# Kernel optimization log

Hardware: AMD Instinct MI355X
Metric: run time of the kernel (lower is better)

## Reference

```python
import jax, jax.numpy as jnp
import numpy as np

ROI_SIZE = 14  # hard-coded in the torch module


def _bilinear(feature, x, y):
    """feature: [B,C,H,W]; x, y: arbitrary (matching) shape S of sample coords.
    Returns [B, C, *S]. Matches torch code: corner indices are clamped BEFORE
    the interpolation weights are computed from them."""
    H, W = feature.shape[-2:]
    y1 = jnp.clip(jnp.floor(y).astype(jnp.int32), 0, H - 1)
    y2 = jnp.clip(jnp.floor(y).astype(jnp.int32) + 1, 0, H - 1)
    x1 = jnp.clip(jnp.floor(x).astype(jnp.int32), 0, W - 1)
    x2 = jnp.clip(jnp.floor(x).astype(jnp.int32) + 1, 0, W - 1)
    wx_lo = x - x1  # weight toward x2 column
    wx_hi = x2 - x  # weight toward x1 column
    wy_lo = y - y1
    wy_hi = y2 - y
    p = feature[:, :, y1, x1] * wx_hi + feature[:, :, y1, x2] * wx_lo
    q = feature[:, :, y2, x1] * wx_hi + feature[:, :, y2, x2] * wx_lo
    return p * wy_hi + q * wy_lo


def setup_inputs() -> dict:
    key = jax.random.key(0)
    kf, k1, k2, k3, k4 = jax.random.split(key, 5)
    B, C, H, W, R = 1, 256, 200, 320, 128
    feature = jax.random.normal(kf, (B, C, H, W), dtype=jnp.float32)
    y1 = jax.random.uniform(k1, (R,), minval=0.0, maxval=H * 0.5)
    x1 = jax.random.uniform(k2, (R,), minval=0.0, maxval=W * 0.5)
    hh = jax.random.uniform(k3, (R,), minval=8.0, maxval=H * 0.45)
    ww = jax.random.uniform(k4, (R,), minval=8.0, maxval=W * 0.45)
    rois = jnp.stack([y1, x1, y1 + hh, x1 + ww], axis=-1).astype(jnp.float32)
    return {"feature": feature, "rois": rois}


def reference(feature, rois):
    R = rois.shape[0]
    B, C, H, W = feature.shape
    sh = (rois[:, 2] - rois[:, 0]) / ROI_SIZE  # [R] bin height stride
    sw = (rois[:, 3] - rois[:, 1]) / ROI_SIZE  # [R] bin width stride
    m = jnp.arange(ROI_SIZE, dtype=rois.dtype)
    y_base = rois[:, 0:1] + sh[:, None] * m  # [R, M]
    x_base = rois[:, 1:2] + sw[:, None] * m  # [R, N]
    frac = jnp.array([1.0 / 3.0, 2.0 / 3.0], dtype=rois.dtype)
    ys = y_base[:, :, None] + sh[:, None, None] * frac  # [R, M, 2]
    xs = x_base[:, :, None] + sw[:, None, None] * frac  # [R, N, 2]
    # all 4 (y, x) sample-point combos per bin -> [R, M, N, 2, 2]
    yy = jnp.broadcast_to(ys[:, :, None, :, None], (R, ROI_SIZE, ROI_SIZE, 2, 2))
    xx = jnp.broadcast_to(xs[:, None, :, None, :], (R, ROI_SIZE, ROI_SIZE, 2, 2))
    samples = _bilinear(feature, xx, yy)  # [B, C, R, M, N, 2, 2]
    # Faithful to torch.max(tensor) with NO dim: global max over B, C, R and
    # the 4 sample points, giving one scalar per bin (m, n).
    bin_max = jnp.max(samples, axis=(0, 1, 2, 5, 6))  # [M, N]
    return jnp.broadcast_to(bin_max, (R, C, ROI_SIZE, ROI_SIZE))
```

## Files before the change

kernel.cpp:

```cpp
#include <hip/hip_runtime.h>
#include <float.h>

#define CC 256
#define HH 200
#define WW 320
#define HW (HH * WW)
#define MM 14
#define SPAN 148
#define NCH 8
#define CG 2
#define CPB (CC / CG)
#define ROUNDS (CPB / NCH)

typedef __attribute__((address_space(1))) const float GF;
typedef __attribute__((address_space(3))) float LF;

__global__ void roi_init(float* __restrict__ binmax) {
    int t = blockIdx.x * blockDim.x + threadIdx.x;
    if (t < MM * MM) binmax[t] = -FLT_MAX;
}

__device__ inline void atomicMaxF(float* addr, float val) {
    if (val >= 0.0f) {
        atomicMax((int*)addr, __float_as_int(val));
    } else {
        atomicMin((unsigned int*)addr, __float_as_uint(val));
    }
}

__global__ __launch_bounds__(256, 4) void roi_reduce(
    const float* __restrict__ feature,
    const float* __restrict__ rois,
    float* __restrict__ binmax)
{
    __shared__ float tile[2][NCH][4][SPAN];
    __shared__ float pmax[4][MM];

    const int bid = blockIdx.x;
    const int cg  = bid & (CG - 1);
    const int rm  = bid >> 1;
    const int m   = rm % MM;
    const int r   = rm / MM;
    const int tid  = threadIdx.x;
    const int w    = tid >> 6;
    const int lane = tid & 63;
    const int cbase = cg * CPB;

    const float ry1 = rois[r * 4 + 0];
    const float rx1 = rois[r * 4 + 1];
    const float ry2 = rois[r * 4 + 2];
    const float rx2 = rois[r * 4 + 3];
    const float sh = (ry2 - ry1) * (1.0f / 14.0f);
    const float sw = (rx2 - rx1) * (1.0f / 14.0f);
    const float f13 = 1.0f / 3.0f, f23 = 2.0f / 3.0f;

    const float yA = ry1 + sh * (float)m + sh * f13;
    const float yB = ry1 + sh * (float)m + sh * f23;
    const int y1A = min(max((int)floorf(yA), 0), HH - 1);
    const int y2A = min(max((int)floorf(yA) + 1, 0), HH - 1);
    const int y1B = min(max((int)floorf(yB), 0), HH - 1);
    const int y2B = min(max((int)floorf(yB) + 1, 0), HH - 1);
    const float wyloA = yA - (float)y1A, wyhiA = (float)y2A - yA;
    const float wyloB = yB - (float)y1B, wyhiB = (float)y2B - yB;

    const float xmin = rx1 + sw * f13;
    const float xmax = rx1 + sw * 13.0f + sw * f23;
    const int xlo = (min(max((int)floorf(xmin), 0), WW - 1)) & ~3;
    const int xhi = min(max((int)floorf(xmax) + 1, 0), WW - 1);
    int span = xhi - xlo + 1;
    if (span > SPAN) span = SPAN;
    const int nlanes = (span + 3) >> 2;

    const int myrow = (w == 0) ? y1A : (w == 1) ? y2A : (w == 2) ? y1B : y2B;
    const float* gbase = feature + (cbase * HW + myrow * WW + xlo) + lane * 4;

    const bool active = lane < 56;
    const int n = lane >> 2;
    const int j = (lane >> 1) & 1;
    const int i = lane & 1;

    float wxlo = 0.f, wxhi = 0.f, wylo = 0.f, wyhi = 0.f;
    int c0 = 0, ra = 0;
    if (active) {
        float x = rx1 + sw * (float)n + sw * (j ? f23 : f13);
        int x1c = min(max((int)floorf(x), 0), WW - 1);
        int x2c = min(max((int)floorf(x) + 1, 0), WW - 1);
        wxlo = x - (float)x1c;
        wxhi = (float)x2c - x;
        c0 = min(max(x1c - xlo, 0), SPAN - 2);
        if (i == 0) { ra = 0; wylo = wyloA; wyhi = wyhiA; }
        else        { ra = 2; wylo = wyloB; wyhi = wyhiB; }
    }

    auto stage = [&](int rd, int b) {
        const float* g = gbase + rd * (NCH * HW);
        if (lane < nlanes) {
            #pragma unroll
            for (int ch = 0; ch < NCH; ++ch) {
                __builtin_amdgcn_global_load_lds(
                    (GF*)(g + ch * HW), (LF*)&tile[b][ch][w][0], 16, 0, 0);
            }
        }
    };

    stage(0, 0);
    float lmax = -FLT_MAX;
    int buf = 0;

    for (int rd = 0; rd < ROUNDS; ++rd) {
        __syncthreads();
        if (rd + 1 < ROUNDS) stage(rd + 1, buf ^ 1);
        if (active) {
            #pragma unroll
            for (int q = 0; q < 2; ++q) {
                const float* rp = &tile[buf][w * 2 + q][ra][0];
                float v11 = rp[c0];
                float v12 = rp[c0 + 1];
                float v21 = rp[SPAN + c0];
                float v22 = rp[SPAN + c0 + 1];
                float p  = v11 * wxhi + v12 * wxlo;
                float qq = v21 * wxhi + v22 * wxlo;
                lmax = fmaxf(lmax, p * wyhi + qq * wylo);
            }
        }
        buf ^= 1;
    }

    float v = lmax;
    v = fmaxf(v, __shfl_xor(v, 1));
    v = fmaxf(v, __shfl_xor(v, 2));
    if (active && (lane & 3) == 0) pmax[w][n] = v;
    __syncthreads();
    if (tid < MM) {
        float vv = fmaxf(fmaxf(pmax[0][tid], pmax[1][tid]),
                         fmaxf(pmax[2][tid], pmax[3][tid]));
        atomicMaxF(&binmax[m * MM + tid], vv);
    }
}

__global__ __launch_bounds__(256) void roi_bcast(
    const float* __restrict__ binmax, float4* __restrict__ out, int total4)
{
    __shared__ float4 b4[49];
    int t = threadIdx.x;
    if (t < 49) b4[t] = ((const float4*)binmax)[t];
    __syncthreads();
    int idx = blockIdx.x * 256 + t;
    if (idx < total4) out[idx] = b4[idx % 49];
}

extern "C" void kernel_launch(void* const* d_in, const int* in_sizes, int n_in,
                              void* d_out, int out_size, void* d_ws, size_t ws_size,
                              hipStream_t stream) {
    const float* feature = (const float*)d_in[0];
    const float* rois    = (const float*)d_in[1];
    float* binmax = (float*)d_ws;
    float* out    = (float*)d_out;

    const int R = in_sizes[1] / 4;

    roi_init<<<1, 256, 0, stream>>>(binmax);
    roi_reduce<<<R * MM * CG, 256, 0, stream>>>(feature, rois, binmax);

    const int total4 = out_size / 4;
    roi_bcast<<<(total4 + 255) / 256, 256, 0, stream>>>(binmax, (float4*)out, total4);
}
```

Baseline: 165.4 us.

## Give each wave private channel slices and pipeline with waitcnt instead of barriers

Each wave now handles its own strided set of 64 channels and loads all four sample rows into a private double-buffered LDS tile. This replaces block-wide __syncthreads with per-wave s_waitcnt vmcnt/lgkmcnt fences. The channel-group split across blocks is removed, which halves the grid and makes each block do more work. The aim is to drop barrier stalls and let the waves stream independently, at the cost of fewer blocks, less occupancy and reliance on hand-written counter fencing.

```diff
diff --git a/kernel.cpp b/kernel.cpp
--- a/kernel.cpp
+++ b/kernel.cpp
@@ -6,11 +6,9 @@
 #define WW 320
 #define HW (HH * WW)
 #define MM 14
-#define SPAN 148
-#define NCH 8
-#define CG 2
-#define CPB (CC / CG)
-#define ROUNDS (CPB / NCH)
+#define SPAN 152
+#define NB 2
+#define CPW 64
 
 typedef __attribute__((address_space(1))) const float GF;
 typedef __attribute__((address_space(3))) float LF;
@@ -28,23 +26,20 @@
     }
 }
 
-__global__ __launch_bounds__(256, 4) void roi_reduce(
+__global__ __launch_bounds__(256) void roi_reduce(
     const float* __restrict__ feature,
     const float* __restrict__ rois,
     float* __restrict__ binmax)
 {
-    __shared__ float tile[2][NCH][4][SPAN];
+    __shared__ float tile[4][NB][4][SPAN];
     __shared__ float pmax[4][MM];
 
     const int bid = blockIdx.x;
-    const int cg  = bid & (CG - 1);
-    const int rm  = bid >> 1;
-    const int m   = rm % MM;
-    const int r   = rm / MM;
+    const int m   = bid % MM;
+    const int r   = bid / MM;
     const int tid  = threadIdx.x;
     const int w    = tid >> 6;
     const int lane = tid & 63;
-    const int cbase = cg * CPB;
 
     const float ry1 = rois[r * 4 + 0];
     const float rx1 = rois[r * 4 + 1];
@@ -71,8 +66,11 @@
     if (span > SPAN) span = SPAN;
     const int nlanes = (span + 3) >> 2;
 
-    const int myrow = (w == 0) ? y1A : (w == 1) ? y2A : (w == 2) ? y1B : y2B;
-    const float* gbase = feature + (cbase * HW + myrow * WW + xlo) + lane * 4;
+    const int rows[4] = { y1A, y2A, y1B, y2B };
+    const float* bp0 = feature + (w * HW + rows[0] * WW + xlo) + lane * 4;
+    const float* bp1 = feature + (w * HW + rows[1] * WW + xlo) + lane * 4;
+    const float* bp2 = feature + (w * HW + rows[2] * WW + xlo) + lane * 4;
+    const float* bp3 = feature + (w * HW + rows[3] * WW + xlo) + lane * 4;
 
     const bool active = lane < 56;
     const int n = lane >> 2;
@@ -80,51 +78,61 @@
     const int i = lane & 1;
 
     float wxlo = 0.f, wxhi = 0.f, wylo = 0.f, wyhi = 0.f;
-    int c0 = 0, ra = 0;
+    int o_lane = 0;
     if (active) {
         float x = rx1 + sw * (float)n + sw * (j ? f23 : f13);
         int x1c = min(max((int)floorf(x), 0), WW - 1);
         int x2c = min(max((int)floorf(x) + 1, 0), WW - 1);
         wxlo = x - (float)x1c;
         wxhi = (float)x2c - x;
-        c0 = min(max(x1c - xlo, 0), SPAN - 2);
-        if (i == 0) { ra = 0; wylo = wyloA; wyhi = wyhiA; }
-        else        { ra = 2; wylo = wyloB; wyhi = wyhiB; }
+        int c0 = min(max(x1c - xlo, 0), SPAN - 2);
+        int ra = i * 2;
+        o_lane = ra * SPAN + c0;
+        if (i == 0) { wylo = wyloA; wyhi = wyhiA; }
+        else        { wylo = wyloB; wyhi = wyhiB; }
     }
+    const float* rp0 = &tile[w][0][0][0] + o_lane;
+    const float* rp1 = &tile[w][1][0][0] + o_lane;
 
-    auto stage = [&](int rd, int b) {
-        const float* g = gbase + rd * (NCH * HW);
+    auto stage = [&](int t, int b) {
+        const int co = t * 4 * HW;
         if (lane < nlanes) {
-            #pragma unroll
-            for (int ch = 0; ch < NCH; ++ch) {
-                __builtin_amdgcn_global_load_lds(
-                    (GF*)(g + ch * HW), (LF*)&tile[b][ch][w][0], 16, 0, 0);
-            }
+            __builtin_amdgcn_global_load_lds((GF*)(bp0 + co), (LF*)&tile[w][b][0][0], 16, 0, 0);
+            __builtin_amdgcn_global_load_lds((GF*)(bp1 + co), (LF*)&tile[w][b][1][0], 16, 0, 0);
+            __builtin_amdgcn_global_load_lds((GF*)(bp2 + co), (LF*)&tile[w][b][2][0], 16, 0, 0);
+            __builtin_amdgcn_global_load_lds((GF*)(bp3 + co), (LF*)&tile[w][b][3][0], 16, 0, 0);
         }
     };
 
+    float lmax = -FLT_MAX;
+    auto compute = [&](const float* rp) {
+        float v11 = rp[0];
+        float v12 = rp[1];
+        float v21 = rp[SPAN];
+        float v22 = rp[SPAN + 1];
+        float p  = v11 * wxhi + v12 * wxlo;
+        float qq = v21 * wxhi + v22 * wxlo;
+        lmax = fmaxf(lmax, p * wyhi + qq * wylo);
+    };
+
     stage(0, 0);
-    float lmax = -FLT_MAX;
-    int buf = 0;
+    stage(1, 1);
 
-    for (int rd = 0; rd < ROUNDS; ++rd) {
-        __syncthreads();
-        if (rd + 1 < ROUNDS) stage(rd + 1, buf ^ 1);
-        if (active) {
-            #pragma unroll
-            for (int q = 0; q < 2; ++q) {
-                const float* rp = &tile[buf][w * 2 + q][ra][0];
-                float v11 = rp[c0];
-                float v12 = rp[c0 + 1];
-                float v21 = rp[SPAN + c0];
-                float v22 = rp[SPAN + c0 + 1];
-                float p  = v11 * wxhi + v12 * wxlo;
-                float qq = v21 * wxhi + v22 * wxlo;
-                lmax = fmaxf(lmax, p * wyhi + qq * wylo);
-            }
-        }
-        buf ^= 1;
+    int t = 0;
+    for (; t + 2 < CPW; t += 2) {
+        asm volatile("s_waitcnt vmcnt(4)" ::: "memory");
+        if (active) compute(rp0);
+        asm volatile("s_waitcnt lgkmcnt(0)" ::: "memory");
+        stage(t + 2, 0);
+        asm volatile("s_waitcnt vmcnt(4)" ::: "memory");
+        if (active) compute(rp1);
+        asm volatile("s_waitcnt lgkmcnt(0)" ::: "memory");
+        stage(t + 3, 1);
     }
+    asm volatile("s_waitcnt vmcnt(4)" ::: "memory");
+    if (active) compute(rp0);
+    asm volatile("s_waitcnt vmcnt(0)" ::: "memory");
+    if (active) compute(rp1);
 
     float v = lmax;
     v = fmaxf(v, __shfl_xor(v, 1));
@@ -160,7 +168,7 @@
     const int R = in_sizes[1] / 4;
 
     roi_init<<<1, 256, 0, stream>>>(binmax);
-    roi_reduce<<<R * MM * CG, 256, 0, stream>>>(feature, rois, binmax);
+    roi_reduce<<<R * MM, 256, 0, stream>>>(feature, rois, binmax);
 
     const int total4 = out_size / 4;
     roi_bcast<<<(total4 + 255) / 256, 256, 0, stream>>>(binmax, (float4*)out, total4);
```

Result: no change. 164.2 us (-0.7%).

## Replace LDS row staging with direct per-sample gathers and grid-stride broadcast

Applied to the files above, without the earlier changes.

The reduction kernel no longer stages whole feature row spans into shared memory with async global-to-LDS loads and double buffering. Each lane now gathers its four bilinear corner values directly from global memory for 8 channels held in registers, with the channel dimension split across 8 groups instead of 2. This cuts the bytes fetched to only the needed corners and removes per-round barriers, at the cost of scattered uncoalesced loads. The broadcast kernel is also changed to a fixed grid of 784 blocks where each thread writes 8 float4 values with a stride, and reads binmax directly without LDS.

```diff
diff --git a/kernel.cpp b/kernel.cpp
--- a/kernel.cpp
+++ b/kernel.cpp
@@ -6,14 +6,9 @@
 #define WW 320
 #define HW (HH * WW)
 #define MM 14
-#define SPAN 148
-#define NCH 8
-#define CG 2
+#define CG 8
 #define CPB (CC / CG)
-#define ROUNDS (CPB / NCH)
-
-typedef __attribute__((address_space(1))) const float GF;
-typedef __attribute__((address_space(3))) float LF;
+#define CPW (CPB / 4)
 
 __global__ void roi_init(float* __restrict__ binmax) {
     int t = blockIdx.x * blockDim.x + threadIdx.x;
@@ -28,23 +23,21 @@
     }
 }
 
-__global__ __launch_bounds__(256, 4) void roi_reduce(
+__global__ __launch_bounds__(256) void roi_reduce(
     const float* __restrict__ feature,
     const float* __restrict__ rois,
     float* __restrict__ binmax)
 {
-    __shared__ float tile[2][NCH][4][SPAN];
     __shared__ float pmax[4][MM];
 
     const int bid = blockIdx.x;
     const int cg  = bid & (CG - 1);
-    const int rm  = bid >> 1;
+    const int rm  = bid >> 3;
     const int m   = rm % MM;
     const int r   = rm / MM;
     const int tid  = threadIdx.x;
     const int w    = tid >> 6;
     const int lane = tid & 63;
-    const int cbase = cg * CPB;
 
     const float ry1 = rois[r * 4 + 0];
     const float rx1 = rois[r * 4 + 1];
@@ -54,82 +47,51 @@
     const float sw = (rx2 - rx1) * (1.0f / 14.0f);
     const float f13 = 1.0f / 3.0f, f23 = 2.0f / 3.0f;
 
-    const float yA = ry1 + sh * (float)m + sh * f13;
-    const float yB = ry1 + sh * (float)m + sh * f23;
-    const int y1A = min(max((int)floorf(yA), 0), HH - 1);
-    const int y2A = min(max((int)floorf(yA) + 1, 0), HH - 1);
-    const int y1B = min(max((int)floorf(yB), 0), HH - 1);
-    const int y2B = min(max((int)floorf(yB) + 1, 0), HH - 1);
-    const float wyloA = yA - (float)y1A, wyhiA = (float)y2A - yA;
-    const float wyloB = yB - (float)y1B, wyhiB = (float)y2B - yB;
+    const int s = lane & 31;
+    const int i = lane >> 5;
+    const int n = s >> 1;
+    const int j = s & 1;
+    const bool active = s < 28;
 
-    const float xmin = rx1 + sw * f13;
-    const float xmax = rx1 + sw * 13.0f + sw * f23;
-    const int xlo = (min(max((int)floorf(xmin), 0), WW - 1)) & ~3;
-    const int xhi = min(max((int)floorf(xmax) + 1, 0), WW - 1);
-    int span = xhi - xlo + 1;
-    if (span > SPAN) span = SPAN;
-    const int nlanes = (span + 3) >> 2;
+    const float x = rx1 + sw * (float)n + sw * (j ? f23 : f13);
+    const float y = ry1 + sh * (float)m + sh * (i ? f23 : f13);
+    const int x1c = min(max((int)floorf(x), 0), WW - 1);
+    const int x2c = min(max((int)floorf(x) + 1, 0), WW - 1);
+    const int y1c = min(max((int)floorf(y), 0), HH - 1);
+    const int y2c = min(max((int)floorf(y) + 1, 0), HH - 1);
+    const float wxlo = x - (float)x1c, wxhi = (float)x2c - x;
+    const float wylo = y - (float)y1c, wyhi = (float)y2c - y;
 
-    const int myrow = (w == 0) ? y1A : (w == 1) ? y2A : (w == 2) ? y1B : y2B;
-    const float* gbase = feature + (cbase * HW + myrow * WW + xlo) + lane * 4;
+    int o11 = y1c * WW + x1c;
+    int o12 = y1c * WW + x2c;
+    int o21 = y2c * WW + x1c;
+    int o22 = y2c * WW + x2c;
+    if (!active) { o11 = o12 = o21 = o22 = 0; }
 
-    const bool active = lane < 56;
-    const int n = lane >> 2;
-    const int j = (lane >> 1) & 1;
-    const int i = lane & 1;
+    const float* fbase = feature + (cg * CPB + w * CPW) * HW;
 
-    float wxlo = 0.f, wxhi = 0.f, wylo = 0.f, wyhi = 0.f;
-    int c0 = 0, ra = 0;
-    if (active) {
-        float x = rx1 + sw * (float)n + sw * (j ? f23 : f13);
-        int x1c = min(max((int)floorf(x), 0), WW - 1);
-        int x2c = min(max((int)floorf(x) + 1, 0), WW - 1);
-        wxlo = x - (float)x1c;
-        wxhi = (float)x2c - x;
-        c0 = min(max(x1c - xlo, 0), SPAN - 2);
-        if (i == 0) { ra = 0; wylo = wyloA; wyhi = wyhiA; }
-        else        { ra = 2; wylo = wyloB; wyhi = wyhiB; }
+    float v11[CPW], v12[CPW], v21[CPW], v22[CPW];
+    #pragma unroll
+    for (int c = 0; c < CPW; ++c) {
+        const float* fc = fbase + c * HW;
+        v11[c] = fc[o11];
+        v12[c] = fc[o12];
+        v21[c] = fc[o21];
+        v22[c] = fc[o22];
     }
 
-    auto stage = [&](int rd, int b) {
-        const float* g = gbase + rd * (NCH * HW);
-        if (lane < nlanes) {
-            #pragma unroll
-            for (int ch = 0; ch < NCH; ++ch) {
-                __builtin_amdgcn_global_load_lds(
-                    (GF*)(g + ch * HW), (LF*)&tile[b][ch][w][0], 16, 0, 0);
-            }
-        }
-    };
-
-    stage(0, 0);
     float lmax = -FLT_MAX;
-    int buf = 0;
-
-    for (int rd = 0; rd < ROUNDS; ++rd) {
-        __syncthreads();
-        if (rd + 1 < ROUNDS) stage(rd + 1, buf ^ 1);
-        if (active) {
-            #pragma unroll
-            for (int q = 0; q < 2; ++q) {
-                const float* rp = &tile[buf][w * 2 + q][ra][0];
-                float v11 = rp[c0];
-                float v12 = rp[c0 + 1];
-                float v21 = rp[SPAN + c0];
-                float v22 = rp[SPAN + c0 + 1];
-                float p  = v11 * wxhi + v12 * wxlo;
-                float qq = v21 * wxhi + v22 * wxlo;
-                lmax = fmaxf(lmax, p * wyhi + qq * wylo);
-            }
-        }
-        buf ^= 1;
+    #pragma unroll
+    for (int c = 0; c < CPW; ++c) {
+        float p = v11[c] * wxhi + v12[c] * wxlo;
+        float q = v21[c] * wxhi + v22[c] * wxlo;
+        lmax = fmaxf(lmax, p * wyhi + q * wylo);
     }
 
     float v = lmax;
     v = fmaxf(v, __shfl_xor(v, 1));
-    v = fmaxf(v, __shfl_xor(v, 2));
-    if (active && (lane & 3) == 0) pmax[w][n] = v;
+    v = fmaxf(v, __shfl_xor(v, 32));
+    if (active && j == 0 && i == 0) pmax[w][n] = v;
     __syncthreads();
     if (tid < MM) {
         float vv = fmaxf(fmaxf(pmax[0][tid], pmax[1][tid]),
@@ -138,15 +100,18 @@
     }
 }
 
+#define BCAST_BLOCKS 784
 __global__ __launch_bounds__(256) void roi_bcast(
     const float* __restrict__ binmax, float4* __restrict__ out, int total4)
 {
-    __shared__ float4 b4[49];
-    int t = threadIdx.x;
-    if (t < 49) b4[t] = ((const float4*)binmax)[t];
-    __syncthreads();
-    int idx = blockIdx.x * 256 + t;
-    if (idx < total4) out[idx] = b4[idx % 49];
+    const int idx0 = blockIdx.x * 256 + threadIdx.x;
+    const float4 val = ((const float4*)binmax)[idx0 % 49];
+    const int stride = BCAST_BLOCKS * 256;
+    #pragma unroll
+    for (int k = 0; k < 8; ++k) {
+        int idx = idx0 + k * stride;
+        if (idx < total4) out[idx] = val;
+    }
 }
 
 extern "C" void kernel_launch(void* const* d_in, const int* in_sizes, int n_in,
@@ -163,5 +128,5 @@
     roi_reduce<<<R * MM * CG, 256, 0, stream>>>(feature, rois, binmax);
 
     const int total4 = out_size / 4;
-    roi_bcast<<<(total4 + 255) / 256, 256, 0, stream>>>(binmax, (float4*)out, total4);
+    roi_bcast<<<BCAST_BLOCKS, 256, 0, stream>>>(binmax, (float4*)out, total4);
 }
```

Measured after the change: 152.5 us. 7.8% less time.
